# Kernel tuning notes

Hardware: AMD Instinct MI355X
Metric: run time of the kernel (lower is better)

Reference implementation:

```python
import jax, jax.numpy as jnp
import numpy as np

WS = 14            # window height/width
CLS = 1            # cls tokens
DIM = 768
H = 12             # heads
DH = DIM // H      # head dim = 64
B = 128
N = WS * WS + CLS  # 197
SCALE = DH ** (-0.5)
TABLE = (2 * WS - 1) ** 2 + CLS  # 730


def _rel_index():
    # Swin-style relative position index, with CLS rows/cols pointing at the
    # last table entry (torch uses index -1 which wraps to TABLE-1).
    c = np.arange(WS)
    coords = np.stack(np.meshgrid(c, c, indexing='ij'))      # [2,14,14]
    cf = coords.reshape(2, -1)                                # [2,196]
    rel = cf[:, :, None] - cf[:, None, :]                     # [2,196,196]
    rel = rel.transpose(1, 2, 0).astype(np.int64)             # [196,196,2]
    rel[..., 0] += WS - 1
    rel[..., 1] += WS - 1
    rel[..., 0] *= 2 * WS - 1
    idx = rel.sum(-1)                                         # [196,196]
    full = np.full((N, N), -1, np.int64)
    full[CLS:, CLS:] = idx
    full = np.where(full < 0, TABLE - 1, full)
    return jnp.asarray(full, jnp.int32)


def setup_inputs() -> dict:
    key = jax.random.key(0)
    ks = jax.random.split(key, 5)
    return {
        'x': jax.random.normal(ks[0], (B, N, DIM), jnp.float32),
        'qkv_w': jax.random.normal(ks[1], (3 * DIM, DIM), jnp.float32) * 0.02,
        'proj_w': jax.random.normal(ks[2], (DIM, DIM), jnp.float32) * 0.02,
        'proj_b': jnp.zeros((DIM,), jnp.float32),
        'bias_table': jax.random.normal(ks[3], (TABLE, H), jnp.float32) * 0.02,
        'rel_idx': _rel_index(),
    }


def reference(x, qkv_w, proj_w, proj_b, bias_table, rel_idx):
    Bc, Nc, C = x.shape
    qkv = x @ qkv_w.T                                   # [B,N,3C]
    qkv = qkv.reshape(Bc, Nc, 3, H, DH).transpose(2, 0, 3, 1, 4)
    q, k, v = qkv[0], qkv[1], qkv[2]                    # [B,H,N,D]
    attn = jnp.einsum('bhnd,bhmd->bhnm', q, k) * SCALE  # [B,H,N,N]
    bias = bias_table[rel_idx]                          # [N,N,H]
    attn = attn + bias.transpose(2, 0, 1)[None]         # broadcast over batch
    attn = jax.nn.softmax(attn, axis=-1)
    out = jnp.einsum('bhnm,bhmd->bhnd', attn, v)        # [B,H,N,D]
    out = out.transpose(0, 2, 1, 3).reshape(Bc, Nc, C)
    return out @ proj_w.T + proj_b
```

## Files before the change

kernel.cpp:

```cpp
#include <hip/hip_runtime.h>
#include <hip/hip_bf16.h>

typedef _Float16 half8 __attribute__((ext_vector_type(8)));
typedef _Float16 half4 __attribute__((ext_vector_type(4)));
typedef float floatx4 __attribute__((ext_vector_type(4)));

#define MFMA16(a, b, c) __builtin_amdgcn_mfma_f32_16x16x32_f16(a, b, c, 0, 0, 0)
#define GLDS16(gp, lp) __builtin_amdgcn_global_load_lds( \
    (const __attribute__((address_space(1))) void*)(gp), \
    (__attribute__((address_space(3))) void*)(lp), 16, 0, 0)

#define BATCH 128
#define NTOK 197
#define DIM 768
#define NH 12
#define DH 64
#define M_ROWS (BATCH * NTOK)
#define KPAD 224
#define NKT 13
#define NTILES (BATCH * NH * NKT)

__global__ void cvt_f32_f16(const float* __restrict__ src, _Float16* __restrict__ dst, int n4) {
    int i = blockIdx.x * 256 + threadIdx.x;
    if (i < n4) {
        float4 v = ((const float4*)src)[i];
        half4 o;
        o[0] = (_Float16)v.x; o[1] = (_Float16)v.y;
        o[2] = (_Float16)v.z; o[3] = (_Float16)v.w;
        ((half4*)dst)[i] = o;
    }
}

__global__ void bias_pre(const float* __restrict__ table, const int* __restrict__ ridx,
                         _Float16* __restrict__ biasph) {
    int idx = blockIdx.x * 256 + threadIdx.x;
    if (idx >= NH * 13 * 13 * 256) return;
    int e = idx & 255;
    int r = e >> 4, q = (e >> 2) & 3, rr = e & 3;
    int t = idx >> 8;
    int nt = t % 13; int t2 = t / 13; int qt = t2 % 13; int h = t2 / 13;
    int row = qt * 16 + q * 4 + rr;
    int col = nt * 16 + r;
    float v = -30000.0f;
    if (col < NTOK) {
        int rc = row < NTOK ? row : NTOK - 1;
        v = table[ridx[rc * NTOK + col] * NH + h];
    }
    biasph[idx] = (_Float16)v;
}

__device__ __forceinline__ void gemm_core_768(const _Float16* __restrict__ A,
                                              const _Float16* __restrict__ B,
                                              int m0b, int n0b,
                                              _Float16* As, _Float16* Bs,
                                              floatx4 acc[4][4]) {
    const int lane = threadIdx.x & 63;
    const int w = threadIdx.x >> 6;
    const int r = lane & 15, q = lane >> 4;
    const int mo = (w & 1) * 64;
    const int no = (w >> 1) * 64;
    const int srow = w * 32 + (lane >> 3);
    const int gatom = (lane & 7) ^ (lane >> 3);
    const int rx = r & 7;

    const _Float16* pa[4];
    const _Float16* pb[4];
#pragma unroll
    for (int c = 0; c < 4; ++c) {
        pa[c] = A + (size_t)(m0b + srow + c * 8) * DIM + gatom * 8;
        pb[c] = B + (size_t)(n0b + srow + c * 8) * DIM + gatom * 8;
    }
    _Float16* ldsA = As + w * 2048;
    _Float16* ldsB = Bs + w * 2048;

    for (int kk = 0; kk < DIM / 64; ++kk) {
#pragma unroll
        for (int c = 0; c < 4; ++c) {
            GLDS16(pa[c], ldsA + c * 512);
            GLDS16(pb[c], ldsB + c * 512);
            pa[c] += 64;
            pb[c] += 64;
        }
        __syncthreads();
#pragma unroll
        for (int s = 0; s < 2; ++s) {
            half8 a[4], b[4];
#pragma unroll
            for (int i = 0; i < 4; ++i)
                a[i] = *(const half8*)&As[((mo + i * 16 + r) * 8 + ((s * 4 + q) ^ rx)) * 8];
#pragma unroll
            for (int j = 0; j < 4; ++j)
                b[j] = *(const half8*)&Bs[((no + j * 16 + r) * 8 + ((s * 4 + q) ^ rx)) * 8];
#pragma unroll
            for (int i = 0; i < 4; ++i)
#pragma unroll
                for (int j = 0; j < 4; ++j)
                    acc[i][j] = MFMA16(a[i], b[j], acc[i][j]);
        }
        __syncthreads();
    }
}

__global__ __launch_bounds__(256) void qkv_gemm(const _Float16* __restrict__ X,
                                                const _Float16* __restrict__ W,
                                                _Float16* __restrict__ qh,
                                                _Float16* __restrict__ kh,
                                                _Float16* __restrict__ vt) {
    __shared__ __align__(16) _Float16 As[128 * 64];
    __shared__ __align__(16) _Float16 Bs[128 * 64];
    const int lane = threadIdx.x & 63;
    const int w = threadIdx.x >> 6;
    const int r = lane & 15, q = lane >> 4;

    floatx4 acc[4][4] = {};
    gemm_core_768(X, W, blockIdx.y * 128, blockIdx.x * 128, As, Bs, acc);

    const int m0 = blockIdx.y * 128 + (w & 1) * 64;
    const int n0 = blockIdx.x * 128 + (w >> 1) * 64;
    const int which = n0 / 768;
    const int hh = (n0 % 768) / 64;
    if (which < 2) {
        _Float16* dst = (which == 0) ? qh : kh;
        const float scale = (which == 0) ? 0.125f : 1.0f;
#pragma unroll
        for (int i = 0; i < 4; ++i) {
#pragma unroll
            for (int rr = 0; rr < 4; ++rr) {
                int grow = m0 + i * 16 + q * 4 + rr;
                int b_idx = grow / 197;
                int n_idx = grow - b_idx * 197;
                size_t rowoff = ((size_t)(b_idx * NH + hh) * NTOK + n_idx) * DH;
#pragma unroll
                for (int j = 0; j < 4; ++j)
                    dst[rowoff + j * 16 + r] = (_Float16)(acc[i][j][rr] * scale);
            }
        }
    } else {
#pragma unroll
        for (int i = 0; i < 4; ++i) {
#pragma unroll
            for (int rr = 0; rr < 4; ++rr) {
                int grow = m0 + i * 16 + q * 4 + rr;
                int b_idx = grow / 197;
                int n_idx = grow - b_idx * 197;
                size_t hbase = (size_t)(b_idx * NH + hh) * DH;
#pragma unroll
                for (int j = 0; j < 4; ++j)
                    vt[(hbase + j * 16 + r) * KPAD + n_idx] = (_Float16)acc[i][j][rr];
            }
        }
    }
}

__global__ __launch_bounds__(256) void proj_gemm(const _Float16* __restrict__ A,
                                                 const _Float16* __restrict__ W,
                                                 const float* __restrict__ bias,
                                                 float* __restrict__ out) {
    __shared__ __align__(16) _Float16 As[128 * 64];
    __shared__ __align__(16) _Float16 Bs[128 * 64];
    const int lane = threadIdx.x & 63;
    const int w = threadIdx.x >> 6;
    const int r = lane & 15, q = lane >> 4;

    floatx4 acc[4][4] = {};
    gemm_core_768(A, W, blockIdx.y * 128, blockIdx.x * 128, As, Bs, acc);

    const int m0 = blockIdx.y * 128 + (w & 1) * 64;
    const int n0 = blockIdx.x * 128 + (w >> 1) * 64;
#pragma unroll
    for (int i = 0; i < 4; ++i) {
#pragma unroll
        for (int rr = 0; rr < 4; ++rr) {
            size_t grow = m0 + i * 16 + q * 4 + rr;
#pragma unroll
            for (int j = 0; j < 4; ++j) {
                int gcol = n0 + j * 16 + r;
                out[grow * DIM + gcol] = acc[i][j][rr] + bias[gcol];
            }
        }
    }
}

__global__ __launch_bounds__(256) void attn_kernel(const _Float16* __restrict__ qh,
                                                   const _Float16* __restrict__ kh,
                                                   const _Float16* __restrict__ vt,
                                                   const _Float16* __restrict__ biasph,
                                                   _Float16* __restrict__ ah) {
    __shared__ __align__(16) _Float16 P[4][16][40];
    const int w = threadIdx.x >> 6, lane = threadIdx.x & 63;
    const int r = lane & 15, q = lane >> 4;
    const int T = blockIdx.x * 4 + w;
    const int bh = T / 13;
    const int qt = T - bh * 13;
    const int b = bh / NH, h = bh - b * NH;
    const _Float16* Qb = qh + (size_t)bh * NTOK * DH;
    const _Float16* Kb = kh + (size_t)bh * NTOK * DH;
    const _Float16* Vtb = vt + (size_t)bh * DH * KPAD;

    half4 bf[NKT];
    const _Float16* bbase = biasph + (((size_t)h * 13 + qt) * 13) * 256 + r * 16 + q * 4;
#pragma unroll
    for (int nt = 0; nt < NKT; ++nt)
        bf[nt] = *(const half4*)(bbase + nt * 256);

    const int rowq = qt * 16 + r;
    half8 aq0 = *(const half8*)(Qb + (size_t)rowq * DH + q * 8);
    half8 aq1 = *(const half8*)(Qb + (size_t)rowq * DH + 32 + q * 8);

    floatx4 sacc[NKT] = {};
#pragma unroll
    for (int nt = 0; nt < NKT; ++nt) {
        half8 b0 = {}, b1 = {};
        int rowk = nt * 16 + r;
        if (rowk < NTOK) {
            b0 = *(const half8*)(Kb + (size_t)rowk * DH + q * 8);
            b1 = *(const half8*)(Kb + (size_t)rowk * DH + 32 + q * 8);
        }
        sacc[nt] = MFMA16(aq0, b0, sacc[nt]);
        sacc[nt] = MFMA16(aq1, b1, sacc[nt]);
    }

    _Float16 pv[NKT][4];
#pragma unroll
    for (int rr = 0; rr < 4; ++rr) {
        float sv[NKT];
        float mx = -3.0e38f;
#pragma unroll
        for (int nt = 0; nt < NKT; ++nt) {
            float s = sacc[nt][rr] + (float)bf[nt][rr];
            sv[nt] = s;
            mx = fmaxf(mx, s);
        }
#pragma unroll
        for (int m = 1; m <= 8; m <<= 1) mx = fmaxf(mx, __shfl_xor(mx, m, 64));
        float sm = 0.f;
#pragma unroll
        for (int nt = 0; nt < NKT; ++nt) {
            float e = __expf(sv[nt] - mx);
            sv[nt] = e;
            sm += e;
        }
#pragma unroll
        for (int m = 1; m <= 8; m <<= 1) sm += __shfl_xor(sm, m, 64);
        float inv = 1.0f / sm;
#pragma unroll
        for (int nt = 0; nt < NKT; ++nt)
            pv[nt][rr] = (_Float16)(sv[nt] * inv);
    }

    floatx4 oacc[4] = {};
    _Float16* Pw = &P[w][0][0];
#pragma unroll
    for (int kt = 0; kt < 7; ++kt) {
        const int nt0 = kt * 2, nt1 = kt * 2 + 1;
#pragma unroll
        for (int rr = 0; rr < 4; ++rr) {
            Pw[(q * 4 + rr) * 40 + r] = pv[nt0][rr];
            Pw[(q * 4 + rr) * 40 + 16 + r] = (nt1 < NKT) ? pv[nt1][rr] : (_Float16)0.0f;
        }
        __asm__ volatile("" ::: "memory");
        half8 ap = *(const half8*)&Pw[r * 40 + q * 8];
        __asm__ volatile("" ::: "memory");
#pragma unroll
        for (int dt = 0; dt < 4; ++dt) {
            half8 bv = *(const half8*)(Vtb + (size_t)(dt * 16 + r) * KPAD + kt * 32 + q * 8);
            oacc[dt] = MFMA16(ap, bv, oacc[dt]);
        }
    }

#pragma unroll
    for (int rr = 0; rr < 4; ++rr) {
        int row = qt * 16 + q * 4 + rr;
        if (row < NTOK) {
            size_t o = ((size_t)b * NTOK + row) * DIM + h * DH;
#pragma unroll
            for (int dt = 0; dt < 4; ++dt)
                ah[o + dt * 16 + r] = (_Float16)oacc[dt][rr];
        }
    }
}

extern "C" void kernel_launch(void* const* d_in, const int* in_sizes, int n_in,
                              void* d_out, int out_size, void* d_ws, size_t ws_size,
                              hipStream_t stream) {
    const float* x = (const float*)d_in[0];
    const float* qkv_w = (const float*)d_in[1];
    const float* proj_w = (const float*)d_in[2];
    const float* proj_b = (const float*)d_in[3];
    const float* table = (const float*)d_in[4];
    const int* ridx = (const int*)d_in[5];
    float* out = (float*)d_out;

    char* ws = (char*)d_ws;
    const size_t SZ_X = (size_t)M_ROWS * DIM * 2;
    const size_t SZ_WQKV = (size_t)3 * DIM * DIM * 2;
    const size_t SZ_WPROJ = (size_t)DIM * DIM * 2;
    const size_t SZ_HEAD = (size_t)BATCH * NH * NTOK * DH * 2;
    const size_t SZ_VT = (size_t)BATCH * NH * DH * KPAD * 2;
    const size_t SZ_BIAS = (size_t)NH * 13 * 13 * 256 * 2;

    _Float16* xh = (_Float16*)(ws + 0);
    _Float16* ah = (_Float16*)(ws + 0);
    _Float16* wqkvh = (_Float16*)(ws + SZ_X);
    _Float16* wprojh = (_Float16*)(ws + SZ_X + SZ_WQKV);
    _Float16* qh = (_Float16*)(ws + SZ_X + SZ_WQKV + SZ_WPROJ);
    _Float16* kh = (_Float16*)(ws + SZ_X + SZ_WQKV + SZ_WPROJ + SZ_HEAD);
    _Float16* vt = (_Float16*)(ws + SZ_X + SZ_WQKV + SZ_WPROJ + 2 * SZ_HEAD);
    _Float16* biasph = (_Float16*)(ws + SZ_X + SZ_WQKV + SZ_WPROJ + 2 * SZ_HEAD + SZ_VT);
    (void)SZ_BIAS; (void)ws_size; (void)n_in; (void)in_sizes; (void)out_size;

    {
        int n4 = M_ROWS * DIM / 4;
        cvt_f32_f16<<<(n4 + 255) / 256, 256, 0, stream>>>(x, xh, n4);
        n4 = 3 * DIM * DIM / 4;
        cvt_f32_f16<<<(n4 + 255) / 256, 256, 0, stream>>>(qkv_w, wqkvh, n4);
        n4 = DIM * DIM / 4;
        cvt_f32_f16<<<(n4 + 255) / 256, 256, 0, stream>>>(proj_w, wprojh, n4);
    }
    {
        int n = NH * 13 * 13 * 256;
        bias_pre<<<(n + 255) / 256, 256, 0, stream>>>(table, ridx, biasph);
    }
    {
        dim3 grid(3 * DIM / 128, M_ROWS / 128);
        qkv_gemm<<<grid, 256, 0, stream>>>(xh, wqkvh, qh, kh, vt);
    }
    attn_kernel<<<NTILES / 4, 256, 0, stream>>>(qh, kh, vt, biasph, ah);
    {
        dim3 grid(DIM / 128, M_ROWS / 128);
        proj_gemm<<<grid, 256, 0, stream>>>(ah, wprojh, proj_b, out);
    }
}
```

Baseline: 468.6 us.

## Pad tokens to 208 and stage QKV epilogue through LDS for vector stores

Input X is converted into a per-batch token layout padded to 208 rows, so each GEMM tile maps onto whole padded rows and Q/K are stored with a padded stride. The QKV GEMM epilogue now transposes accumulators through shared memory and writes 16-byte half8 vectors to Q, K and the transposed V, replacing scattered 2-byte stores. The attention kernel drops the K-row bounds check because padded rows exist. This adds about 5% extra GEMM rows and an LDS round trip with a barrier, in exchange for coalesced stores and simpler index math.

Result: faster. 454.5 us (-3.0%).

```diff
diff --git a/kernel.cpp b/kernel.cpp
--- a/kernel.cpp
+++ b/kernel.cpp
@@ -12,10 +12,12 @@
 
 #define BATCH 128
 #define NTOK 197
+#define NPAD 208
 #define DIM 768
 #define NH 12
 #define DH 64
 #define M_ROWS (BATCH * NTOK)
+#define MP_ROWS (BATCH * NPAD)
 #define KPAD 224
 #define NKT 13
 #define NTILES (BATCH * NH * NKT)
@@ -29,6 +31,24 @@
         o[2] = (_Float16)v.z; o[3] = (_Float16)v.w;
         ((half4*)dst)[i] = o;
     }
+}
+
+__global__ void cvt_x_pad(const float* __restrict__ src, _Float16* __restrict__ dst) {
+    int idx = blockIdx.x * 256 + threadIdx.x;
+    if (idx >= MP_ROWS * (DIM / 8)) return;
+    int row = idx / (DIM / 8), ch = idx - row * (DIM / 8);
+    int b = row / NPAD, n = row - b * NPAD;
+    half8 o = {};
+    if (n < NTOK) {
+        const float* s = src + (size_t)(b * NTOK + n) * DIM + ch * 8;
+        float4 v0 = *(const float4*)s;
+        float4 v1 = *(const float4*)(s + 4);
+        o[0] = (_Float16)v0.x; o[1] = (_Float16)v0.y;
+        o[2] = (_Float16)v0.z; o[3] = (_Float16)v0.w;
+        o[4] = (_Float16)v1.x; o[5] = (_Float16)v1.y;
+        o[6] = (_Float16)v1.z; o[7] = (_Float16)v1.w;
+    }
+    *(half8*)&dst[(size_t)row * DIM + ch * 8] = o;
 }
 
 __global__ void bias_pre(const float* __restrict__ table, const int* __restrict__ ridx,
@@ -106,48 +126,72 @@
                                                 _Float16* __restrict__ qh,
                                                 _Float16* __restrict__ kh,
                                                 _Float16* __restrict__ vt) {
-    __shared__ __align__(16) _Float16 As[128 * 64];
-    __shared__ __align__(16) _Float16 Bs[128 * 64];
+    __shared__ __align__(16) _Float16 smem[17408];
+    _Float16* As = smem;
+    _Float16* Bs = smem + 8192;
     const int lane = threadIdx.x & 63;
     const int w = threadIdx.x >> 6;
     const int r = lane & 15, q = lane >> 4;
+    const int m0b = blockIdx.y * 128;
+    const int n0b = blockIdx.x * 128;
 
     floatx4 acc[4][4] = {};
-    gemm_core_768(X, W, blockIdx.y * 128, blockIdx.x * 128, As, Bs, acc);
-
-    const int m0 = blockIdx.y * 128 + (w & 1) * 64;
-    const int n0 = blockIdx.x * 128 + (w >> 1) * 64;
-    const int which = n0 / 768;
-    const int hh = (n0 % 768) / 64;
-    if (which < 2) {
+    gemm_core_768(X, W, m0b, n0b, As, Bs, acc);
+
+    const int which = n0b / 768;
+    const int gw = (w & 1) * 64;
+    const int cw = (w >> 1) * 64;
+    _Float16* T = smem;
+
+    if (which == 2) {
+#pragma unroll
+        for (int i = 0; i < 4; ++i) {
+#pragma unroll
+            for (int j = 0; j < 4; ++j) {
+                half4 hv;
+#pragma unroll
+                for (int rr = 0; rr < 4; ++rr) hv[rr] = (_Float16)acc[i][j][rr];
+                *(half4*)&T[(cw + j * 16 + r) * 136 + gw + i * 16 + q * 4] = hv;
+            }
+        }
+    } else {
+        const float scale = (which == 0) ? 0.125f : 1.0f;
+#pragma unroll
+        for (int i = 0; i < 4; ++i)
+#pragma unroll
+            for (int j = 0; j < 4; ++j)
+#pragma unroll
+                for (int rr = 0; rr < 4; ++rr)
+                    T[(gw + i * 16 + q * 4 + rr) * 136 + cw + j * 16 + r] =
+                        (_Float16)(acc[i][j][rr] * scale);
+    }
+    __syncthreads();
+
+    const int t = threadIdx.x;
+    if (which == 2) {
+#pragma unroll
+        for (int p = 0; p < 8; ++p) {
+            int idx = p * 256 + t;
+            int c = idx >> 4, g0 = (idx & 15) * 8;
+            int grow = m0b + g0;
+            int b_idx = grow / NPAD, n_idx = grow - b_idx * NPAD;
+            int vcol = n0b + c - 1536;
+            int hh = vcol >> 6, d = vcol & 63;
+            half8 hv = *(const half8*)&T[c * 136 + g0];
+            *(half8*)&vt[((size_t)(b_idx * NH + hh) * DH + d) * KPAD + n_idx] = hv;
+        }
+    } else {
         _Float16* dst = (which == 0) ? qh : kh;
-        const float scale = (which == 0) ? 0.125f : 1.0f;
-#pragma unroll
-        for (int i = 0; i < 4; ++i) {
-#pragma unroll
-            for (int rr = 0; rr < 4; ++rr) {
-                int grow = m0 + i * 16 + q * 4 + rr;
-                int b_idx = grow / 197;
-                int n_idx = grow - b_idx * 197;
-                size_t rowoff = ((size_t)(b_idx * NH + hh) * NTOK + n_idx) * DH;
-#pragma unroll
-                for (int j = 0; j < 4; ++j)
-                    dst[rowoff + j * 16 + r] = (_Float16)(acc[i][j][rr] * scale);
-            }
-        }
-    } else {
-#pragma unroll
-        for (int i = 0; i < 4; ++i) {
-#pragma unroll
-            for (int rr = 0; rr < 4; ++rr) {
-                int grow = m0 + i * 16 + q * 4 + rr;
-                int b_idx = grow / 197;
-                int n_idx = grow - b_idx * 197;
-                size_t hbase = (size_t)(b_idx * NH + hh) * DH;
-#pragma unroll
-                for (int j = 0; j < 4; ++j)
-                    vt[(hbase + j * 16 + r) * KPAD + n_idx] = (_Float16)acc[i][j][rr];
-            }
+#pragma unroll
+        for (int p = 0; p < 8; ++p) {
+            int idx = p * 256 + t;
+            int g = idx >> 4, c0 = (idx & 15) * 8;
+            int grow = m0b + g;
+            int b_idx = grow / NPAD, n_idx = grow - b_idx * NPAD;
+            int colm = (n0b + c0) % 768;
+            int hh = colm >> 6, d0 = colm & 63;
+            half8 hv = *(const half8*)&T[g * 136 + c0];
+            *(half8*)&dst[((size_t)(b_idx * NH + hh) * NPAD + n_idx) * DH + d0] = hv;
         }
     }
 }
@@ -193,8 +237,8 @@
     const int bh = T / 13;
     const int qt = T - bh * 13;
     const int b = bh / NH, h = bh - b * NH;
-    const _Float16* Qb = qh + (size_t)bh * NTOK * DH;
-    const _Float16* Kb = kh + (size_t)bh * NTOK * DH;
+    const _Float16* Qb = qh + (size_t)bh * NPAD * DH;
+    const _Float16* Kb = kh + (size_t)bh * NPAD * DH;
     const _Float16* Vtb = vt + (size_t)bh * DH * KPAD;
 
     half4 bf[NKT];
@@ -210,12 +254,9 @@
     floatx4 sacc[NKT] = {};
 #pragma unroll
     for (int nt = 0; nt < NKT; ++nt) {
-        half8 b0 = {}, b1 = {};
         int rowk = nt * 16 + r;
-        if (rowk < NTOK) {
-            b0 = *(const half8*)(Kb + (size_t)rowk * DH + q * 8);
-            b1 = *(const half8*)(Kb + (size_t)rowk * DH + 32 + q * 8);
-        }
+        half8 b0 = *(const half8*)(Kb + (size_t)rowk * DH + q * 8);
+        half8 b1 = *(const half8*)(Kb + (size_t)rowk * DH + 32 + q * 8);
         sacc[nt] = MFMA16(aq0, b0, sacc[nt]);
         sacc[nt] = MFMA16(aq1, b1, sacc[nt]);
     }
@@ -292,27 +333,27 @@
     float* out = (float*)d_out;
 
     char* ws = (char*)d_ws;
-    const size_t SZ_X = (size_t)M_ROWS * DIM * 2;
+    const size_t SZ_XP = (size_t)MP_ROWS * DIM * 2;
     const size_t SZ_WQKV = (size_t)3 * DIM * DIM * 2;
     const size_t SZ_WPROJ = (size_t)DIM * DIM * 2;
-    const size_t SZ_HEAD = (size_t)BATCH * NH * NTOK * DH * 2;
+    const size_t SZ_QK = (size_t)BATCH * NH * NPAD * DH * 2;
     const size_t SZ_VT = (size_t)BATCH * NH * DH * KPAD * 2;
     const size_t SZ_BIAS = (size_t)NH * 13 * 13 * 256 * 2;
 
     _Float16* xh = (_Float16*)(ws + 0);
     _Float16* ah = (_Float16*)(ws + 0);
-    _Float16* wqkvh = (_Float16*)(ws + SZ_X);
-    _Float16* wprojh = (_Float16*)(ws + SZ_X + SZ_WQKV);
-    _Float16* qh = (_Float16*)(ws + SZ_X + SZ_WQKV + SZ_WPROJ);
-    _Float16* kh = (_Float16*)(ws + SZ_X + SZ_WQKV + SZ_WPROJ + SZ_HEAD);
-    _Float16* vt = (_Float16*)(ws + SZ_X + SZ_WQKV + SZ_WPROJ + 2 * SZ_HEAD);
-    _Float16* biasph = (_Float16*)(ws + SZ_X + SZ_WQKV + SZ_WPROJ + 2 * SZ_HEAD + SZ_VT);
+    _Float16* wqkvh = (_Float16*)(ws + SZ_XP);
+    _Float16* wprojh = (_Float16*)(ws + SZ_XP + SZ_WQKV);
+    _Float16* qh = (_Float16*)(ws + SZ_XP + SZ_WQKV + SZ_WPROJ);
+    _Float16* kh = (_Float16*)(ws + SZ_XP + SZ_WQKV + SZ_WPROJ + SZ_QK);
+    _Float16* vt = (_Float16*)(ws + SZ_XP + SZ_WQKV + SZ_WPROJ + 2 * SZ_QK);
+    _Float16* biasph = (_Float16*)(ws + SZ_XP + SZ_WQKV + SZ_WPROJ + 2 * SZ_QK + SZ_VT);
     (void)SZ_BIAS; (void)ws_size; (void)n_in; (void)in_sizes; (void)out_size;
 
     {
-        int n4 = M_ROWS * DIM / 4;
-        cvt_f32_f16<<<(n4 + 255) / 256, 256, 0, stream>>>(x, xh, n4);
-        n4 = 3 * DIM * DIM / 4;
+        int nc = MP_ROWS * (DIM / 8);
+        cvt_x_pad<<<(nc + 255) / 256, 256, 0, stream>>>(x, xh);
+        int n4 = 3 * DIM * DIM / 4;
         cvt_f32_f16<<<(n4 + 255) / 256, 256, 0, stream>>>(qkv_w, wqkvh, n4);
         n4 = DIM * DIM / 4;
         cvt_f32_f16<<<(n4 + 255) / 256, 256, 0, stream>>>(proj_w, wprojh, n4);
@@ -322,7 +363,7 @@
         bias_pre<<<(n + 255) / 256, 256, 0, stream>>>(table, ridx, biasph);
     }
     {
-        dim3 grid(3 * DIM / 128, M_ROWS / 128);
+        dim3 grid(3 * DIM / 128, MP_ROWS / 128);
         qkv_gemm<<<grid, 256, 0, stream>>>(xh, wqkvh, qh, kh, vt);
     }
     attn_kernel<<<NTILES / 4, 256, 0, stream>>>(qh, kh, vt, biasph, ah);
```
